# Kernel tuning notes

Measured on AMD Instinct MI355X. Metric: run time of the kernel, lower is better.

## Reference

```python
import jax, jax.numpy as jnp
import numpy as np

IN_FEATURES = 4096
OUT_FEATURES = 4096
INQ = IN_FEATURES // 4
OUTQ = OUT_FEATURES // 4


def setup_inputs() -> dict:
    key = jax.random.key(0)
    kx, krr, kri, krj, krk, kb = jax.random.split(key, 6)
    scale = 1.0 / np.sqrt(INQ)
    x = jax.random.normal(kx, (8192, IN_FEATURES), dtype=jnp.float32)
    W_rr = jax.random.uniform(krr, (OUTQ, INQ), jnp.float32, -scale, scale)
    # ri/rj/rk weights are scaled by 0.5 at init in the original module
    W_ri = jax.random.uniform(kri, (OUTQ, INQ), jnp.float32, -scale, scale) * 0.5
    W_rj = jax.random.uniform(krj, (OUTQ, INQ), jnp.float32, -scale, scale) * 0.5
    W_rk = jax.random.uniform(krk, (OUTQ, INQ), jnp.float32, -scale, scale) * 0.5
    b_rr = jax.random.uniform(kb, (OUTQ,), jnp.float32, -scale, scale)
    return {"x": x, "W_rr": W_rr, "W_ri": W_ri, "W_rj": W_rj, "W_rk": W_rk, "b_rr": b_rr}


def reference(x, W_rr, W_ri, W_rj, W_rk, b_rr):
    B, F = x.shape
    q = F // 4
    # Stack the four quaternion components: Xc[c] = component c, shape (4, B, q)
    Xc = x.reshape(B, 4, q).transpose(1, 0, 2)
    # Apply each quarter-sized linear to all four components at once.
    Rr = jnp.einsum('cbi,oi->cbo', Xc, W_rr) + b_rr  # linear_rr (with bias)
    Ri = jnp.einsum('cbi,oi->cbo', Xc, W_ri)         # linear_ri
    Rj = jnp.einsum('cbi,oi->cbo', Xc, W_rj)         # linear_rj
    Rk = jnp.einsum('cbi,oi->cbo', Xc, W_rk)         # linear_rk
    # Hamilton-product style combination
    out_r = Rr[0] - Ri[1] - Rj[2] - Rk[3]
    out_i = Ri[0] + Rr[1] + Rk[2] - Rj[3]
    out_j = Rj[0] - Rk[1] + Rr[2] + Ri[3]
    out_k = Rk[0] + Rj[1] - Ri[2] + Rr[3]
    # torch.stack(dim=1).view(B,-1) == concat along features
    return jnp.concatenate([out_r, out_i, out_j, out_k], axis=1)
```

## Files before the change

kernel.cpp:

```cpp
#include <hip/hip_runtime.h>
#include <hip/hip_bf16.h>
#include <stdint.h>

#define M_DIM 8192
#define K_DIM 4096
#define N_DIM 4096
#define QO 1024
#define BM 256
#define BN 128
#define BK 32
#define FBM 128
#define FBN 128

typedef __bf16 bf16x8_t __attribute__((ext_vector_type(8)));
typedef float f32x4_t __attribute__((ext_vector_type(4)));

__device__ __forceinline__ uint32_t f2bf_rne(float f) {
    union { float f; uint32_t u; } v; v.f = f;
    return (v.u + 0x7FFFu + ((v.u >> 16) & 1u)) >> 16;
}
__device__ __forceinline__ uint32_t pack2bf(float lo, float hi) {
    return f2bf_rne(lo) | (f2bf_rne(hi) << 16);
}

__global__ __launch_bounds__(256) void cvt_x_kernel(const float* __restrict__ x,
                                                    uint16_t* __restrict__ xb, int n8) {
    int i = blockIdx.x * 256 + threadIdx.x;
    if (i >= n8) return;
    float4 v0 = ((const float4*)x)[2 * i];
    float4 v1 = ((const float4*)x)[2 * i + 1];
    uint4 o;
    o.x = pack2bf(v0.x, v0.y);
    o.y = pack2bf(v0.z, v0.w);
    o.z = pack2bf(v1.x, v1.y);
    o.w = pack2bf(v1.z, v1.w);
    ((uint4*)xb)[i] = o;
}

__global__ __launch_bounds__(256) void build_w_kernel(
    const float* __restrict__ wrr, const float* __restrict__ wri,
    const float* __restrict__ wrj, const float* __restrict__ wrk,
    uint16_t* __restrict__ wb, int n8) {
    int g = blockIdx.x * 256 + threadIdx.x;
    if (g >= n8) return;
    int n  = g >> 9;
    int k8 = (g & 511) << 3;
    int cp = n >> 10, o = n & 1023;
    int c  = k8 >> 10, i = k8 & 1023;
    int tsel = cp ^ c;
    const float* w = (tsel == 0) ? wrr : (tsel == 1) ? wri : (tsel == 2) ? wrj : wrk;
    float s = ((0x428Eu >> ((cp << 2) | c)) & 1u) ? -1.0f : 1.0f;
    const float* p = w + (size_t)o * QO + i;
    float4 v0 = ((const float4*)p)[0];
    float4 v1 = ((const float4*)p)[1];
    uint4 ob;
    ob.x = pack2bf(s * v0.x, s * v0.y);
    ob.y = pack2bf(s * v0.z, s * v0.w);
    ob.z = pack2bf(s * v1.x, s * v1.y);
    ob.w = pack2bf(s * v1.z, s * v1.w);
    ((uint4*)wb)[g] = ob;
}

__global__ __launch_bounds__(256, 2) void qgemm256_kernel(
    const uint16_t* __restrict__ Abf, const uint16_t* __restrict__ Bbf,
    const float* __restrict__ bias, float* __restrict__ C)
{
    __shared__ uint16_t lA[BM * BK];
    __shared__ uint16_t lB[BN * BK];
    const int t    = threadIdx.x;
    const int wave = t >> 6;
    const int lane = t & 63;
    const int bn = blockIdx.x, bm = blockIdx.y;
    const int wm = wave >> 1, wn = wave & 1;

    f32x4_t acc[8][4];
#pragma unroll
    for (int a = 0; a < 8; ++a)
#pragma unroll
        for (int b = 0; b < 4; ++b)
            acc[a][b] = (f32x4_t){0.f, 0.f, 0.f, 0.f};

    const int fr  = lane & 15;
    const int fkb = (lane >> 4) << 3;
    const uint16_t* pA[8];
    const uint16_t* pB[4];
#pragma unroll
    for (int i = 0; i < 8; ++i)
        pA[i] = lA + (wm * 128 + i * 16 + fr) * BK + fkb;
#pragma unroll
    for (int i = 0; i < 4; ++i)
        pB[i] = lB + (wn * 64 + i * 16 + fr) * BK + fkb;

    const int srow = lane >> 2;
    const int scol = (lane & 3) << 3;
    const uint16_t* gA0 = Abf + (size_t)(bm * BM + wave * 64 + srow) * K_DIM + scol;
    const uint16_t* gB0 = Bbf + (size_t)(bn * BN + wave * 32 + srow) * K_DIM + scol;
    uint16_t* lA0 = lA + wave * 64 * BK;
    uint16_t* lB0 = lB + wave * 32 * BK;

#pragma unroll 1
    for (int kb = 0; kb < K_DIM; kb += BK) {
#pragma unroll
        for (int i = 0; i < 4; ++i)
            __builtin_amdgcn_global_load_lds(
                (const __attribute__((address_space(1))) void*)(gA0 + (size_t)i * 16 * K_DIM + kb),
                (__attribute__((address_space(3))) void*)(lA0 + i * 16 * BK), 16, 0, 0);
#pragma unroll
        for (int i = 0; i < 2; ++i)
            __builtin_amdgcn_global_load_lds(
                (const __attribute__((address_space(1))) void*)(gB0 + (size_t)i * 16 * K_DIM + kb),
                (__attribute__((address_space(3))) void*)(lB0 + i * 16 * BK), 16, 0, 0);
        __syncthreads();

        bf16x8_t bfr[4];
#pragma unroll
        for (int i = 0; i < 4; ++i)
            bfr[i] = *(const bf16x8_t*)pB[i];
#pragma unroll
        for (int mi = 0; mi < 8; ++mi) {
            bf16x8_t af = *(const bf16x8_t*)pA[mi];
#pragma unroll
            for (int ni = 0; ni < 4; ++ni)
                acc[mi][ni] = __builtin_amdgcn_mfma_f32_16x16x32_bf16(
                    af, bfr[ni], acc[mi][ni], 0, 0, 0);
        }
        __syncthreads();
    }

    const int row0 = bm * BM + wm * 128 + ((lane >> 4) << 2);
    const int col0 = bn * BN + wn * 64 + (lane & 15);
#pragma unroll
    for (int ni = 0; ni < 4; ++ni) {
        const int col = col0 + ni * 16;
        const float bv = bias[col & (QO - 1)];
#pragma unroll
        for (int mi = 0; mi < 8; ++mi) {
            const int r = row0 + mi * 16;
            float* cptr = C + (size_t)r * N_DIM + col;
#pragma unroll
            for (int rr = 0; rr < 4; ++rr)
                cptr[(size_t)rr * N_DIM] = acc[mi][ni][rr] + bv;
        }
    }
}

__global__ __launch_bounds__(256) void qgemm_fb_kernel(
    const float* __restrict__ x,
    const float* __restrict__ wrr, const float* __restrict__ wri,
    const float* __restrict__ wrj, const float* __restrict__ wrk,
    const float* __restrict__ bias, float* __restrict__ C)
{
    __shared__ uint16_t lA[FBM * BK];
    __shared__ uint16_t lB[FBN * BK];
    const int t    = threadIdx.x;
    const int wave = t >> 6;
    const int lane = t & 63;
    const int bn = blockIdx.x, bm = blockIdx.y;
    const int wm = wave >> 1, wn = wave & 1;

    f32x4_t acc[4][4];
#pragma unroll
    for (int a = 0; a < 4; ++a)
#pragma unroll
        for (int b = 0; b < 4; ++b)
            acc[a][b] = (f32x4_t){0.f, 0.f, 0.f, 0.f};

    const int fr  = lane & 15;
    const int fkb = (lane >> 4) << 3;
    const uint16_t* pA[4];
    const uint16_t* pB[4];
#pragma unroll
    for (int i = 0; i < 4; ++i) {
        pA[i] = lA + (wm * 64 + i * 16 + fr) * BK + fkb;
        pB[i] = lB + (wn * 64 + i * 16 + fr) * BK + fkb;
    }

    const int mr = t >> 1;
    const int mc = (t & 1) << 4;
    int ng = bn * FBN + mr;
    int bcp = ng >> 10;
    int bo  = ng & 1023;

#pragma unroll 1
    for (int kb = 0; kb < K_DIM; kb += BK) {
        const float* pa = x + (size_t)(bm * FBM + mr) * K_DIM + kb + mc;
        float4 a0 = ((const float4*)pa)[0], a1 = ((const float4*)pa)[1],
               a2 = ((const float4*)pa)[2], a3 = ((const float4*)pa)[3];
        uint4 wv0 = make_uint4(pack2bf(a0.x, a0.y), pack2bf(a0.z, a0.w),
                               pack2bf(a1.x, a1.y), pack2bf(a1.z, a1.w));
        uint4 wv1 = make_uint4(pack2bf(a2.x, a2.y), pack2bf(a2.z, a2.w),
                               pack2bf(a3.x, a3.y), pack2bf(a3.z, a3.w));
        *(uint4*)(lA + mr * BK + mc)     = wv0;
        *(uint4*)(lA + mr * BK + mc + 8) = wv1;

        int k0 = kb + mc;
        int c  = k0 >> 10, ii = k0 & 1023;
        int tsel = bcp ^ c;
        const float* w = (tsel == 0) ? wrr : (tsel == 1) ? wri : (tsel == 2) ? wrj : wrk;
        float s = ((0x428Eu >> ((bcp << 2) | c)) & 1u) ? -1.0f : 1.0f;
        const float* pb = w + (size_t)bo * QO + ii;
        float4 b0 = ((const float4*)pb)[0], b1 = ((const float4*)pb)[1],
               b2 = ((const float4*)pb)[2], b3 = ((const float4*)pb)[3];
        uint4 u0 = make_uint4(pack2bf(s * b0.x, s * b0.y), pack2bf(s * b0.z, s * b0.w),
                              pack2bf(s * b1.x, s * b1.y), pack2bf(s * b1.z, s * b1.w));
        uint4 u1 = make_uint4(pack2bf(s * b2.x, s * b2.y), pack2bf(s * b2.z, s * b2.w),
                              pack2bf(s * b3.x, s * b3.y), pack2bf(s * b3.z, s * b3.w));
        *(uint4*)(lB + mr * BK + mc)     = u0;
        *(uint4*)(lB + mr * BK + mc + 8) = u1;
        __syncthreads();

        bf16x8_t af[4], bfr[4];
#pragma unroll
        for (int i = 0; i < 4; ++i) {
            af[i]  = *(const bf16x8_t*)pA[i];
            bfr[i] = *(const bf16x8_t*)pB[i];
        }
#pragma unroll
        for (int mi = 0; mi < 4; ++mi)
#pragma unroll
            for (int ni = 0; ni < 4; ++ni)
                acc[mi][ni] = __builtin_amdgcn_mfma_f32_16x16x32_bf16(
                    af[mi], bfr[ni], acc[mi][ni], 0, 0, 0);
        __syncthreads();
    }

    const int row0 = bm * FBM + wm * 64 + ((lane >> 4) << 2);
    const int col0 = bn * FBN + wn * 64 + (lane & 15);
#pragma unroll
    for (int ni = 0; ni < 4; ++ni) {
        const int col = col0 + ni * 16;
        const float bv = bias[col & (QO - 1)];
#pragma unroll
        for (int mi = 0; mi < 4; ++mi) {
            const int r = row0 + mi * 16;
            float* cptr = C + (size_t)r * N_DIM + col;
#pragma unroll
            for (int rr = 0; rr < 4; ++rr)
                cptr[(size_t)rr * N_DIM] = acc[mi][ni][rr] + bv;
        }
    }
}

extern "C" void kernel_launch(void* const* d_in, const int* in_sizes, int n_in,
                              void* d_out, int out_size, void* d_ws, size_t ws_size,
                              hipStream_t stream) {
    const float* x   = (const float*)d_in[0];
    const float* wrr = (const float*)d_in[1];
    const float* wri = (const float*)d_in[2];
    const float* wrj = (const float*)d_in[3];
    const float* wrk = (const float*)d_in[4];
    const float* brr = (const float*)d_in[5];
    float* out = (float*)d_out;

    const size_t xb_bytes = (size_t)M_DIM * K_DIM * 2;
    const size_t wb_bytes = (size_t)N_DIM * K_DIM * 2;

    if (ws_size >= xb_bytes + wb_bytes) {
        uint16_t* xb = (uint16_t*)d_ws;
        uint16_t* wb = (uint16_t*)((char*)d_ws + xb_bytes);
        const int nx8 = M_DIM * K_DIM / 8;
        cvt_x_kernel<<<nx8 / 256, 256, 0, stream>>>(x, xb, nx8);
        const int nw8 = N_DIM * K_DIM / 8;
        build_w_kernel<<<nw8 / 256, 256, 0, stream>>>(wrr, wri, wrj, wrk, wb, nw8);
        dim3 grid(N_DIM / BN, M_DIM / BM);
        qgemm256_kernel<<<grid, 256, 0, stream>>>(xb, wb, brr, out);
    } else {
        dim3 grid(N_DIM / FBN, M_DIM / FBM);
        qgemm_fb_kernel<<<grid, 256, 0, stream>>>(x, wrr, wri, wrj, wrk, brr, out);
    }
}
```

Baseline: 550.0 us.

## Double-buffer LDS tiles to overlap global loads with MFMA compute

Splits the A and B shared-memory tiles into two buffers. The next K-slice is prefetched with global_load_lds into the spare buffer while MFMAs run on the current one, and each iteration uses a single barrier instead of two. The goal is to hide global-memory latency behind compute. In exchange LDS use doubles, which may cut occupancy. The single barrier may also not wait for the async LDS loads (vmcnt) before the tile is read.

```diff
diff --git a/kernel.cpp b/kernel.cpp
--- a/kernel.cpp
+++ b/kernel.cpp
@@ -65,8 +65,8 @@
     const uint16_t* __restrict__ Abf, const uint16_t* __restrict__ Bbf,
     const float* __restrict__ bias, float* __restrict__ C)
 {
-    __shared__ uint16_t lA[BM * BK];
-    __shared__ uint16_t lB[BN * BK];
+    __shared__ uint16_t lA[2][BM * BK];
+    __shared__ uint16_t lB[2][BN * BK];
     const int t    = threadIdx.x;
     const int wave = t >> 6;
     const int lane = t & 63;
@@ -82,49 +82,58 @@
 
     const int fr  = lane & 15;
     const int fkb = (lane >> 4) << 3;
-    const uint16_t* pA[8];
-    const uint16_t* pB[4];
+    int oA[8], oB[4];
 #pragma unroll
     for (int i = 0; i < 8; ++i)
-        pA[i] = lA + (wm * 128 + i * 16 + fr) * BK + fkb;
+        oA[i] = (wm * 128 + i * 16 + fr) * BK + fkb;
 #pragma unroll
     for (int i = 0; i < 4; ++i)
-        pB[i] = lB + (wn * 64 + i * 16 + fr) * BK + fkb;
+        oB[i] = (wn * 64 + i * 16 + fr) * BK + fkb;
 
     const int srow = lane >> 2;
     const int scol = (lane & 3) << 3;
     const uint16_t* gA0 = Abf + (size_t)(bm * BM + wave * 64 + srow) * K_DIM + scol;
     const uint16_t* gB0 = Bbf + (size_t)(bn * BN + wave * 32 + srow) * K_DIM + scol;
-    uint16_t* lA0 = lA + wave * 64 * BK;
-    uint16_t* lB0 = lB + wave * 32 * BK;
-
-#pragma unroll 1
-    for (int kb = 0; kb < K_DIM; kb += BK) {
+    const int lAo = wave * 64 * BK;
+    const int lBo = wave * 32 * BK;
+
+    auto stage = [&](int kb, int buf) {
 #pragma unroll
         for (int i = 0; i < 4; ++i)
             __builtin_amdgcn_global_load_lds(
                 (const __attribute__((address_space(1))) void*)(gA0 + (size_t)i * 16 * K_DIM + kb),
-                (__attribute__((address_space(3))) void*)(lA0 + i * 16 * BK), 16, 0, 0);
+                (__attribute__((address_space(3))) void*)(&lA[buf][lAo + i * 16 * BK]), 16, 0, 0);
 #pragma unroll
         for (int i = 0; i < 2; ++i)
             __builtin_amdgcn_global_load_lds(
                 (const __attribute__((address_space(1))) void*)(gB0 + (size_t)i * 16 * K_DIM + kb),
-                (__attribute__((address_space(3))) void*)(lB0 + i * 16 * BK), 16, 0, 0);
-        __syncthreads();
-
+                (__attribute__((address_space(3))) void*)(&lB[buf][lBo + i * 16 * BK]), 16, 0, 0);
+    };
+
+    stage(0, 0);
+    __syncthreads();
+
+    int cur = 0;
+#pragma unroll 1
+    for (int kb = 0; kb < K_DIM; kb += BK, cur ^= 1) {
+        const int nkb = kb + BK;
+        if (nkb < K_DIM) stage(nkb, cur ^ 1);
+
+        const uint16_t* bA = lA[cur];
+        const uint16_t* bB = lB[cur];
         bf16x8_t bfr[4];
 #pragma unroll
         for (int i = 0; i < 4; ++i)
-            bfr[i] = *(const bf16x8_t*)pB[i];
+            bfr[i] = *(const bf16x8_t*)(bB + oB[i]);
 #pragma unroll
         for (int mi = 0; mi < 8; ++mi) {
-            bf16x8_t af = *(const bf16x8_t*)pA[mi];
+            bf16x8_t af = *(const bf16x8_t*)(bA + oA[mi]);
 #pragma unroll
             for (int ni = 0; ni < 4; ++ni)
                 acc[mi][ni] = __builtin_amdgcn_mfma_f32_16x16x32_bf16(
                     af, bfr[ni], acc[mi][ni], 0, 0, 0);
         }
-        __syncthreads();
+        if (nkb < K_DIM) __syncthreads();
     }
 
     const int row0 = bm * BM + wm * 128 + ((lane >> 4) << 2);
```

Measured after the change: 552.7 us. Within noise of the previous version (+0.5%).
